# Kernel tuning notes

Hardware: AMD Instinct MI355X
Metric: run time of the kernel (lower is better)

Reference implementation:

```python
import jax, jax.numpy as jnp
import numpy as np

N = 60000      # total nodes
D = 300        # feature dim
R = 5          # num relations == num bases
E = 1_000_000  # edges
S = 25000      # last_idx_senses
G = 50000      # last_idx_globals
BATCH = 32


def setup_inputs() -> dict:
    key = jax.random.key(0)
    ks = jax.random.split(key, 12)
    x = jax.random.normal(ks[0], (N, D), dtype=jnp.float32)
    edge_index = jax.random.randint(ks[1], (2, E), 0, N, dtype=jnp.int32)
    edge_type = jax.random.randint(ks[2], (E,), 0, R, dtype=jnp.int32)
    current_node_index = jax.random.randint(ks[3], (BATCH,), 0, N, dtype=jnp.int32)
    scale = 1.0 / np.sqrt(D)
    # RGCNConv basis decomposition params (num_bases == num_relations)
    basis = jax.random.normal(ks[4], (R, D, D), dtype=jnp.float32) * scale
    comp = jax.random.normal(ks[5], (R, R), dtype=jnp.float32) * scale
    root = jax.random.normal(ks[6], (D, D), dtype=jnp.float32) * scale
    bias = jnp.zeros((D,), dtype=jnp.float32)
    # heads
    w_global = jax.random.normal(ks[7], (G - S, D), dtype=jnp.float32) * scale
    b_global = jnp.zeros((G - S,), dtype=jnp.float32)
    w_sense = jax.random.normal(ks[8], (S, D), dtype=jnp.float32) * scale
    b_sense = jnp.zeros((S,), dtype=jnp.float32)
    return {
        "x": x, "edge_index": edge_index, "edge_type": edge_type,
        "current_node_index": current_node_index,
        "basis": basis, "comp": comp, "root": root, "bias": bias,
        "w_global": w_global, "b_global": b_global,
        "w_sense": w_sense, "b_sense": b_sense,
    }


def reference(x, edge_index, edge_type, current_node_index,
              basis, comp, root, bias,
              w_global, b_global, w_sense, b_sense):
    src, dst = edge_index[0], edge_index[1]
    # Combined segment id over (dst node, relation): mean-aggregate source
    # features per (node, relation), then apply the per-relation transform
    # (mean(x_j) @ W_r == mean(x_j @ W_r); matches PyG RGCNConv aggr='mean').
    seg = dst * R + edge_type                      # [E]
    msg_sum = jax.ops.segment_sum(x[src], seg, num_segments=N * R)  # [N*R, D]
    cnt = jax.ops.segment_sum(jnp.ones((E,), jnp.float32), seg, num_segments=N * R)
    mean = msg_sum.reshape(N, R, D) / jnp.maximum(cnt.reshape(N, R, 1), 1.0)
    # basis decomposition: W_r = sum_b comp[r,b] * basis[b]
    W = jnp.einsum('rb,bij->rij', comp, basis)     # [R, D, D]
    agg = jnp.einsum('nrd,rde->ne', mean, W)       # [N, D]
    h = jax.nn.relu(agg + x @ root + bias)         # [N, D]
    hc = h[current_node_index]                     # [B, D]
    logits_global = hc @ w_global.T + b_global     # [B, G-S]
    logits_sense = hc @ w_sense.T + b_sense        # [B, S]
    return (jax.nn.log_softmax(logits_global, axis=-1),
            jax.nn.log_softmax(logits_sense, axis=-1))
```

## Files before the change

### kernel.cpp

```cpp
#include <hip/hip_runtime.h>
#include <hip/hip_bf16.h>
#include <math.h>

#define NN 60000
#define D 300
#define R 5
#define NE 1000000
#define B 32
#define NG 25000
#define NS 25000
#define NROWS 50000
#define KCH 50
#define NKC 36
#define HCP 304
#define MCAP 1000000

typedef __bf16 bf16x8 __attribute__((ext_vector_type(8)));
typedef float f32x16 __attribute__((ext_vector_type(16)));


__global__ void zero_ws(float4* __restrict__ p) {
    int i = blockIdx.x * 256 + threadIdx.x;
    if (i < 12040) p[i] = float4{0.f, 0.f, 0.f, 0.f};
    if (i == 0) ((int*)p)[53024] = 0;
}

__global__ __launch_bounds__(256) void edge_scan2(
        const int* __restrict__ ei, const int* __restrict__ et,
        const int* __restrict__ cur,
        float* __restrict__ wcnt, int2* __restrict__ mlist, int* __restrict__ mcnt) {
    __shared__ unsigned int tbl[32];
    __shared__ int curl[B];
    int tid = threadIdx.x;
    if (tid < 32) tbl[tid] = 0u;
    __syncthreads();
    if (tid < B) {
        int c = cur[tid];
        curl[tid] = c;
        atomicOr(&tbl[(c >> 5) & 31], 1u << (c & 31));
    }
    __syncthreads();
    long base = ((long)blockIdx.x * 256 + tid) * 4;
    if (base >= NE) return;
    int ds[4];
    if (base + 4 <= NE) {
        int4 d4 = *(const int4*)(ei + NE + base);
        ds[0] = d4.x; ds[1] = d4.y; ds[2] = d4.z; ds[3] = d4.w;
    } else {
        for (int k = 0; k < 4; ++k) ds[k] = (base + k < NE) ? ei[NE + base + k] : -1;
    }
    #pragma unroll
    for (int k = 0; k < 4; ++k) {
        int dst = ds[k];
        if (dst < 0) continue;
        if (!(tbl[(dst >> 5) & 31] & (1u << (dst & 31)))) continue;
        int e = (int)base + k;
        int r = -1, s = 0;
        for (int b = 0; b < B; ++b) {
            if (dst == curl[b]) {
                if (r < 0) { r = et[e]; s = ei[e]; }
                int slot = b * R + r;
                atomicAdd(&wcnt[slot], 1.0f);
                int pos = atomicAdd(mcnt, 1);
                if (pos < MCAP) mlist[pos] = int2{s, slot};
            }
        }
    }
}

__global__ __launch_bounds__(256) void edge_accum(
        const int2* __restrict__ mlist, const int* __restrict__ mcnt,
        const float* __restrict__ x, float* __restrict__ wsum) {
    int n = *mcnt; if (n > MCAP) n = MCAP;
    for (int m = blockIdx.x; m < n; m += gridDim.x) {
        int2 p = mlist[m];
        const float* xs = x + (long)p.x * D;
        float* sm = wsum + (long)p.y * D;
        for (int t = threadIdx.x; t < D; t += 256) atomicAdd(&sm[t], xs[t]);
    }
}

__global__ void stage_u(const float* __restrict__ x, const int* __restrict__ cur,
                        const float* __restrict__ comp,
                        const float* __restrict__ wsum, const float* __restrict__ wcnt,
                        float* __restrict__ U) {
    int b = blockIdx.x, t = threadIdx.x;
    __shared__ float cmp[R * R];
    __shared__ float inv[R];
    if (t < R * R) cmp[t] = comp[t];
    if (t < R) inv[t] = 1.0f / fmaxf(wcnt[b * R + t], 1.0f);
    __syncthreads();
    if (t >= D) return;
    int node = cur[b];
    U[(long)b * 1800 + t] = x[(long)node * D + t];
    float mean[R];
    #pragma unroll
    for (int r = 0; r < R; ++r) mean[r] = wsum[((long)b * R + r) * D + t] * inv[r];
    #pragma unroll
    for (int bb = 0; bb < R; ++bb) {
        float a = 0.f;
        #pragma unroll
        for (int r = 0; r < R; ++r) a = fmaf(cmp[r * R + bb], mean[r], a);
        U[(long)b * 1800 + 300 + bb * 300 + t] = a;
    }
}

__global__ __launch_bounds__(320) void rgcn_part(const float* __restrict__ root,
                                                 const float* __restrict__ basis,
                                                 const float* __restrict__ U,
                                                 float* __restrict__ part) {
    int kc = blockIdx.x, t = threadIdx.x;
    __shared__ float uL[B * KCH];
    int d0 = kc * KCH;
    for (int i = t; i < B * KCH; i += 320) {
        int b = i / KCH, dd = i - b * KCH;
        uL[i] = U[(long)b * 1800 + d0 + dd];
    }
    __syncthreads();
    if (t >= D) return;
    const float* Mbase = (d0 < 300) ? (root + (long)d0 * D) : (basis + (long)(d0 - 300) * D);
    float acc[B] = {};
    #pragma unroll 5
    for (int i = 0; i < KCH; ++i) {
        float m = Mbase[(long)i * D + t];
        #pragma unroll
        for (int b = 0; b < B; ++b) acc[b] = fmaf(uL[b * KCH + i], m, acc[b]);
    }
    for (int b = 0; b < B; ++b) part[((long)kc * B + b) * D + t] = acc[b];
}

__global__ void finish_hc(const float* __restrict__ part, const float* __restrict__ bias,
                          __bf16* __restrict__ hcb) {
    int b = blockIdx.x, t = threadIdx.x;
    if (t >= HCP) return;
    float a = 0.f;
    if (t < D) {
        a = bias[t];
        for (int kc = 0; kc < NKC; ++kc) a += part[((long)kc * B + b) * D + t];
        a = fmaxf(a, 0.f);
    }
    hcb[b * HCP + t] = (__bf16)a;
}

__global__ __launch_bounds__(64) void head_gemm_mfma(
    const __bf16* __restrict__ hcb, const float* __restrict__ wg, const float* __restrict__ bg,
    const float* __restrict__ wsn, const float* __restrict__ bsn, float* __restrict__ out) {
    int l = threadIdx.x;
    int j0 = blockIdx.x * 32;
    int lm = l & 31, lh = l >> 5;

    bf16x8 bfrag[19];
    const __bf16* hrow = hcb + lm * HCP + lh * 8;
    #pragma unroll
    for (int s = 0; s < 19; ++s) bfrag[s] = *(const bf16x8*)(hrow + 16 * s);

    int row = j0 + lm; if (row >= NROWS) row = NROWS - 1;
    const float* wrow = ((row < NG) ? (wg + (long)row * D) : (wsn + (long)(row - NG) * D)) + lh * 8;

    f32x16 acc = {};
    #pragma unroll
    for (int s = 0; s < 18; ++s) {
        float4 w0 = *(const float4*)(wrow + 16 * s);
        float4 w1 = *(const float4*)(wrow + 16 * s + 4);
        bf16x8 a;
        a[0] = (__bf16)w0.x; a[1] = (__bf16)w0.y; a[2] = (__bf16)w0.z; a[3] = (__bf16)w0.w;
        a[4] = (__bf16)w1.x; a[5] = (__bf16)w1.y; a[6] = (__bf16)w1.z; a[7] = (__bf16)w1.w;
        acc = __builtin_amdgcn_mfma_f32_32x32x16_bf16(a, bfrag[s], acc, 0, 0, 0);
    }
    {
        float4 w0, w1;
        if (lh == 0) {
            w0 = *(const float4*)(wrow + 288);
            w1 = *(const float4*)(wrow + 292);
        } else {
            w0 = *(const float4*)(wrow + 288);
            w1 = float4{0.f, 0.f, 0.f, 0.f};
        }
        bf16x8 a;
        a[0] = (__bf16)w0.x; a[1] = (__bf16)w0.y; a[2] = (__bf16)w0.z; a[3] = (__bf16)w0.w;
        a[4] = (__bf16)w1.x; a[5] = (__bf16)w1.y; a[6] = (__bf16)w1.z; a[7] = (__bf16)w1.w;
        acc = __builtin_amdgcn_mfma_f32_32x32x16_bf16(a, bfrag[18], acc, 0, 0, 0);
    }

    int b = lm;
    #pragma unroll
    for (int r = 0; r < 16; ++r) {
        int j = j0 + (r & 3) + 8 * (r >> 2) + 4 * lh;
        if (j >= NROWS) continue;
        float bv = (j < NG) ? bg[j] : bsn[j - NG];
        float* op = (j < NG) ? (out + (long)b * NG + j)
                             : (out + (long)B * NG + (long)b * NS + (j - NG));
        *op = acc[r] + bv;
    }
}

__global__ __launch_bounds__(1024) void log_softmax_rows(float* __restrict__ out) {
    int row = blockIdx.x;
    int head = row >> 5, b = row & 31;
    float* p = out + (long)head * (B * NG) + (long)b * NG;
    float4* p4 = (float4*)p;
    int tid = threadIdx.x;
    __shared__ float red[16];
    float m = -INFINITY;
    for (int i = tid; i < 6250; i += 1024) {
        float4 v = p4[i];
        m = fmaxf(fmaxf(fmaxf(m, v.x), v.y), fmaxf(v.z, v.w));
    }
    #pragma unroll
    for (int o = 32; o; o >>= 1) m = fmaxf(m, __shfl_xor(m, o));
    if ((tid & 63) == 0) red[tid >> 6] = m;
    __syncthreads();
    if (tid == 0) {
        float mm = red[0];
        for (int i = 1; i < 16; ++i) mm = fmaxf(mm, red[i]);
        red[0] = mm;
    }
    __syncthreads();
    m = red[0];
    __syncthreads();
    float s = 0.f;
    for (int i = tid; i < 6250; i += 1024) {
        float4 v = p4[i];
        s += __expf(v.x - m) + __expf(v.y - m) + __expf(v.z - m) + __expf(v.w - m);
    }
    #pragma unroll
    for (int o = 32; o; o >>= 1) s += __shfl_xor(s, o);
    if ((tid & 63) == 0) red[tid >> 6] = s;
    __syncthreads();
    if (tid == 0) {
        float ss = 0.f;
        for (int i = 0; i < 16; ++i) ss += red[i];
        red[0] = m + __logf(ss);
    }
    __syncthreads();
    float lse = red[0];
    for (int i = tid; i < 6250; i += 1024) {
        float4 v = p4[i];
        v.x -= lse; v.y -= lse; v.z -= lse; v.w -= lse;
        p4[i] = v;
    }
}

extern "C" void kernel_launch(void* const* d_in, const int* in_sizes, int n_in,
                              void* d_out, int out_size, void* d_ws, size_t ws_size,
                              hipStream_t stream) {
    const float* x     = (const float*)d_in[0];
    const int*   ei    = (const int*)d_in[1];
    const int*   et    = (const int*)d_in[2];
    const int*   cur   = (const int*)d_in[3];
    const float* basis = (const float*)d_in[4];
    const float* comp  = (const float*)d_in[5];
    const float* root  = (const float*)d_in[6];
    const float* bias  = (const float*)d_in[7];
    const float* wg    = (const float*)d_in[8];
    const float* bgl   = (const float*)d_in[9];
    const float* wsn   = (const float*)d_in[10];
    const float* bsn   = (const float*)d_in[11];
    float* out  = (float*)d_out;
    float* wsf  = (float*)d_ws;
    float* wsum = wsf;
    float* wcnt = wsf + 48000;
    __bf16* hcb = (__bf16*)(wsf + 48160);
    int*   mcnt = (int*)(wsf + 53024);
    int2*  mlist = (int2*)(wsf + 53028);
    float* part = out;
    float* U    = out + 400000;

    zero_ws<<<48, 256, 0, stream>>>((float4*)d_ws);
    edge_scan2<<<977, 256, 0, stream>>>(ei, et, cur, wcnt, mlist, mcnt);
    edge_accum<<<512, 256, 0, stream>>>(mlist, mcnt, x, wsum);
    stage_u<<<B, 320, 0, stream>>>(x, cur, comp, wsum, wcnt, U);
    rgcn_part<<<NKC, 320, 0, stream>>>(root, basis, U, part);
    finish_hc<<<B, 320, 0, stream>>>(part, bias, hcb);
    head_gemm_mfma<<<(NROWS + 31) / 32, 64, 0, stream>>>(hcb, wg, bgl, wsn, bsn, out);
    log_softmax_rows<<<64, 1024, 0, stream>>>(out);
}
```

Before: 75.97 us.

## Fuse edge scan with accumulation, merge RGCN stages, compute softmax stats in GEMM epilogue

The edge scan now keeps matching edges in a per-block shared list and accumulates their source rows straight away, which removes the global match list and the separate accumulate kernel. The mean/basis mixing, partial GEMM and final reduction are merged into one kernel. It reduces over blocks with float atomics and lets the last block finish the job, detected with a done counter. The head GEMM epilogue computes online max/sum partials per 32-column block, so the 1024-thread three-pass log-softmax becomes a small merge plus one subtract pass over many blocks. Kernel launches and full passes over the logits drop, in exchange for atomic contention and a per-block shared list capped at 64 entries that could silently drop edges.

```diff
diff --git a/kernel.cpp b/kernel.cpp
--- a/kernel.cpp
+++ b/kernel.cpp
@@ -10,10 +10,8 @@
 #define NG 25000
 #define NS 25000
 #define NROWS 50000
-#define KCH 50
-#define NKC 36
 #define HCP 304
-#define MCAP 1000000
+#define NBLK 1563
 
 typedef __bf16 bf16x8 __attribute__((ext_vector_type(8)));
 typedef float f32x16 __attribute__((ext_vector_type(16)));
@@ -21,18 +19,20 @@
 
 __global__ void zero_ws(float4* __restrict__ p) {
     int i = blockIdx.x * 256 + threadIdx.x;
-    if (i < 12040) p[i] = float4{0.f, 0.f, 0.f, 0.f};
-    if (i == 0) ((int*)p)[53024] = 0;
-}
-
-__global__ __launch_bounds__(256) void edge_scan2(
+    if (i < 14441) p[i] = float4{0.f, 0.f, 0.f, 0.f};
+}
+
+__global__ __launch_bounds__(256) void scan_accum(
         const int* __restrict__ ei, const int* __restrict__ et,
-        const int* __restrict__ cur,
-        float* __restrict__ wcnt, int2* __restrict__ mlist, int* __restrict__ mcnt) {
+        const int* __restrict__ cur, const float* __restrict__ x,
+        float* __restrict__ wsum, float* __restrict__ wcnt) {
     __shared__ unsigned int tbl[32];
     __shared__ int curl[B];
+    __shared__ int lcnt;
+    __shared__ int2 loc[64];
     int tid = threadIdx.x;
     if (tid < 32) tbl[tid] = 0u;
+    if (tid == 0) lcnt = 0;
     __syncthreads();
     if (tid < B) {
         int c = cur[tid];
@@ -41,110 +41,122 @@
     }
     __syncthreads();
     long base = ((long)blockIdx.x * 256 + tid) * 4;
-    if (base >= NE) return;
-    int ds[4];
-    if (base + 4 <= NE) {
-        int4 d4 = *(const int4*)(ei + NE + base);
-        ds[0] = d4.x; ds[1] = d4.y; ds[2] = d4.z; ds[3] = d4.w;
+    if (base < NE) {
+        int ds[4];
+        if (base + 4 <= NE) {
+            int4 d4 = *(const int4*)(ei + NE + base);
+            ds[0] = d4.x; ds[1] = d4.y; ds[2] = d4.z; ds[3] = d4.w;
+        } else {
+            for (int k = 0; k < 4; ++k) ds[k] = (base + k < NE) ? ei[NE + base + k] : -1;
+        }
+        #pragma unroll
+        for (int k = 0; k < 4; ++k) {
+            int dst = ds[k];
+            if (dst < 0) continue;
+            if (!(tbl[(dst >> 5) & 31] & (1u << (dst & 31)))) continue;
+            int e = (int)base + k;
+            int r = -1, s = 0;
+            for (int b = 0; b < B; ++b) {
+                if (dst == curl[b]) {
+                    if (r < 0) { r = et[e]; s = ei[e]; }
+                    int slot = b * R + r;
+                    atomicAdd(&wcnt[slot], 1.0f);
+                    int p = atomicAdd(&lcnt, 1);
+                    if (p < 64) loc[p] = int2{s, slot};
+                }
+            }
+        }
+    }
+    __syncthreads();
+    int n = lcnt; if (n > 64) n = 64;
+    for (int m = 0; m < n; ++m) {
+        int2 pr = loc[m];
+        const float* xs = x + (long)pr.x * D;
+        float* sm = wsum + (long)pr.y * D;
+        for (int t = tid; t < D; t += 256) atomicAdd(&sm[t], xs[t]);
+    }
+}
+
+__global__ __launch_bounds__(320) void rgcn_hc(
+        const float* __restrict__ x, const int* __restrict__ cur,
+        const float* __restrict__ comp, const float* __restrict__ root,
+        const float* __restrict__ basis, const float* __restrict__ bias,
+        const float* __restrict__ wsum, const float* __restrict__ wcnt,
+        float* __restrict__ hcf, int* __restrict__ done, __bf16* __restrict__ hcb) {
+    int kc = blockIdx.x, t = threadIdx.x;
+    __shared__ float uL[B * 50];
+    __shared__ float cmp[R * R];
+    __shared__ float inv[B * R];
+    __shared__ int curlS[B];
+    __shared__ int lastFlag;
+    if (t < R * R) cmp[t] = comp[t];
+    if (t < B * R) inv[t] = 1.0f / fmaxf(wcnt[t], 1.0f);
+    if (t < B) curlS[t] = cur[t];
+    __syncthreads();
+    int d0 = kc * 50;
+    if (kc < 6) {
+        for (int i = t; i < B * 50; i += 320) {
+            int b = i / 50, dd = i - b * 50;
+            uL[i] = x[(long)curlS[b] * D + d0 + dd];
+        }
     } else {
-        for (int k = 0; k < 4; ++k) ds[k] = (base + k < NE) ? ei[NE + base + k] : -1;
-    }
-    #pragma unroll
-    for (int k = 0; k < 4; ++k) {
-        int dst = ds[k];
-        if (dst < 0) continue;
-        if (!(tbl[(dst >> 5) & 31] & (1u << (dst & 31)))) continue;
-        int e = (int)base + k;
-        int r = -1, s = 0;
-        for (int b = 0; b < B; ++b) {
-            if (dst == curl[b]) {
-                if (r < 0) { r = et[e]; s = ei[e]; }
-                int slot = b * R + r;
-                atomicAdd(&wcnt[slot], 1.0f);
-                int pos = atomicAdd(mcnt, 1);
-                if (pos < MCAP) mlist[pos] = int2{s, slot};
-            }
-        }
-    }
-}
-
-__global__ __launch_bounds__(256) void edge_accum(
-        const int2* __restrict__ mlist, const int* __restrict__ mcnt,
-        const float* __restrict__ x, float* __restrict__ wsum) {
-    int n = *mcnt; if (n > MCAP) n = MCAP;
-    for (int m = blockIdx.x; m < n; m += gridDim.x) {
-        int2 p = mlist[m];
-        const float* xs = x + (long)p.x * D;
-        float* sm = wsum + (long)p.y * D;
-        for (int t = threadIdx.x; t < D; t += 256) atomicAdd(&sm[t], xs[t]);
-    }
-}
-
-__global__ void stage_u(const float* __restrict__ x, const int* __restrict__ cur,
-                        const float* __restrict__ comp,
-                        const float* __restrict__ wsum, const float* __restrict__ wcnt,
-                        float* __restrict__ U) {
-    int b = blockIdx.x, t = threadIdx.x;
-    __shared__ float cmp[R * R];
-    __shared__ float inv[R];
-    if (t < R * R) cmp[t] = comp[t];
-    if (t < R) inv[t] = 1.0f / fmaxf(wcnt[b * R + t], 1.0f);
-    __syncthreads();
-    if (t >= D) return;
-    int node = cur[b];
-    U[(long)b * 1800 + t] = x[(long)node * D + t];
-    float mean[R];
-    #pragma unroll
-    for (int r = 0; r < R; ++r) mean[r] = wsum[((long)b * R + r) * D + t] * inv[r];
-    #pragma unroll
-    for (int bb = 0; bb < R; ++bb) {
+        int g0 = d0 - 300;
+        int bb = g0 / 300, t0 = g0 - bb * 300;
+        for (int i = t; i < B * 50; i += 320) {
+            int b = i / 50, dd = i - b * 50;
+            float a = 0.f;
+            #pragma unroll
+            for (int r = 0; r < R; ++r)
+                a = fmaf(cmp[r * R + bb] * inv[b * R + r], wsum[((long)b * R + r) * D + t0 + dd], a);
+            uL[i] = a;
+        }
+    }
+    __syncthreads();
+    const float* Mb = (kc < 6) ? (root + (long)d0 * D) : (basis + (long)(d0 - 300) * D);
+    if (t < D) {
+        float acc[B] = {};
+        #pragma unroll 5
+        for (int i = 0; i < 50; ++i) {
+            float m = Mb[(long)i * D + t];
+            #pragma unroll
+            for (int b = 0; b < B; ++b) acc[b] = fmaf(uL[b * 50 + i], m, acc[b]);
+        }
+        for (int b = 0; b < B; ++b) atomicAdd(&hcf[b * D + t], acc[b]);
+    }
+    __syncthreads();
+    if (t == 0) {
+        __threadfence();
+        int p = atomicAdd(done, 1);
+        lastFlag = (p == 35);
+    }
+    __syncthreads();
+    if (!lastFlag) return;
+    __threadfence();
+    for (int i = t; i < B * HCP; i += 320) {
+        int b = i / HCP, tt = i - b * HCP;
         float a = 0.f;
-        #pragma unroll
-        for (int r = 0; r < R; ++r) a = fmaf(cmp[r * R + bb], mean[r], a);
-        U[(long)b * 1800 + 300 + bb * 300 + t] = a;
-    }
-}
-
-__global__ __launch_bounds__(320) void rgcn_part(const float* __restrict__ root,
-                                                 const float* __restrict__ basis,
-                                                 const float* __restrict__ U,
-                                                 float* __restrict__ part) {
-    int kc = blockIdx.x, t = threadIdx.x;
-    __shared__ float uL[B * KCH];
-    int d0 = kc * KCH;
-    for (int i = t; i < B * KCH; i += 320) {
-        int b = i / KCH, dd = i - b * KCH;
-        uL[i] = U[(long)b * 1800 + d0 + dd];
-    }
-    __syncthreads();
-    if (t >= D) return;
-    const float* Mbase = (d0 < 300) ? (root + (long)d0 * D) : (basis + (long)(d0 - 300) * D);
-    float acc[B] = {};
-    #pragma unroll 5
-    for (int i = 0; i < KCH; ++i) {
-        float m = Mbase[(long)i * D + t];
-        #pragma unroll
-        for (int b = 0; b < B; ++b) acc[b] = fmaf(uL[b * KCH + i], m, acc[b]);
-    }
-    for (int b = 0; b < B; ++b) part[((long)kc * B + b) * D + t] = acc[b];
-}
-
-__global__ void finish_hc(const float* __restrict__ part, const float* __restrict__ bias,
-                          __bf16* __restrict__ hcb) {
-    int b = blockIdx.x, t = threadIdx.x;
-    if (t >= HCP) return;
-    float a = 0.f;
-    if (t < D) {
-        a = bias[t];
-        for (int kc = 0; kc < NKC; ++kc) a += part[((long)kc * B + b) * D + t];
-        a = fmaxf(a, 0.f);
-    }
-    hcb[b * HCP + t] = (__bf16)a;
+        if (tt < D) {
+            a = atomicAdd(&hcf[b * D + tt], 0.0f) + bias[tt];
+            a = fmaxf(a, 0.f);
+        }
+        hcb[i] = (__bf16)a;
+    }
+}
+
+__device__ inline void online_upd(float& m, float& s, float v) {
+    if (v > m) { s = s * __expf(m - v) + 1.0f; m = v; }
+    else       { s += __expf(v - m); }
+}
+__device__ inline void online_merge(float& m, float& s, float om, float os) {
+    float M = fmaxf(m, om);
+    s = s * __expf(m - M) + os * __expf(om - M);
+    m = M;
 }
 
 __global__ __launch_bounds__(64) void head_gemm_mfma(
     const __bf16* __restrict__ hcb, const float* __restrict__ wg, const float* __restrict__ bg,
-    const float* __restrict__ wsn, const float* __restrict__ bsn, float* __restrict__ out) {
+    const float* __restrict__ wsn, const float* __restrict__ bsn,
+    float* __restrict__ out, float2* __restrict__ pm2) {
     int l = threadIdx.x;
     int j0 = blockIdx.x * 32;
     int lm = l & 31, lh = l >> 5;
@@ -183,61 +195,59 @@
     }
 
     int b = lm;
+    float m0 = -3.0e38f, s0 = 0.f, m1 = -3.0e38f, s1 = 0.f;
     #pragma unroll
     for (int r = 0; r < 16; ++r) {
         int j = j0 + (r & 3) + 8 * (r >> 2) + 4 * lh;
         if (j >= NROWS) continue;
         float bv = (j < NG) ? bg[j] : bsn[j - NG];
+        float v = acc[r] + bv;
         float* op = (j < NG) ? (out + (long)b * NG + j)
                              : (out + (long)B * NG + (long)b * NS + (j - NG));
-        *op = acc[r] + bv;
-    }
-}
-
-__global__ __launch_bounds__(1024) void log_softmax_rows(float* __restrict__ out) {
-    int row = blockIdx.x;
-    int head = row >> 5, b = row & 31;
-    float* p = out + (long)head * (B * NG) + (long)b * NG;
-    float4* p4 = (float4*)p;
+        *op = v;
+        if (j < NG) online_upd(m0, s0, v); else online_upd(m1, s1, v);
+    }
+    float om0 = __shfl_xor(m0, 32), os0 = __shfl_xor(s0, 32);
+    float om1 = __shfl_xor(m1, 32), os1 = __shfl_xor(s1, 32);
+    online_merge(m0, s0, om0, os0);
+    online_merge(m1, s1, om1, os1);
+    if (lh == 0) {
+        pm2[(long)b * NBLK + blockIdx.x]       = float2{m0, s0};
+        pm2[(long)(B + b) * NBLK + blockIdx.x] = float2{m1, s1};
+    }
+}
+
+__global__ __launch_bounds__(256) void sub_lse(float* __restrict__ out,
+                                               const float2* __restrict__ pm2) {
+    int row = blockIdx.x / 25, c = blockIdx.x % 25;
     int tid = threadIdx.x;
-    __shared__ float red[16];
-    float m = -INFINITY;
-    for (int i = tid; i < 6250; i += 1024) {
-        float4 v = p4[i];
-        m = fmaxf(fmaxf(fmaxf(m, v.x), v.y), fmaxf(v.z, v.w));
-    }
-    #pragma unroll
-    for (int o = 32; o; o >>= 1) m = fmaxf(m, __shfl_xor(m, o));
-    if ((tid & 63) == 0) red[tid >> 6] = m;
+    const float2* pr = pm2 + (long)row * NBLK;
+    float m = -3.0e38f, s = 0.f;
+    for (int i = tid; i < NBLK; i += 256) {
+        float2 e = pr[i];
+        online_merge(m, s, e.x, e.y);
+    }
+    #pragma unroll
+    for (int o = 32; o; o >>= 1) {
+        float om = __shfl_xor(m, o), os = __shfl_xor(s, o);
+        online_merge(m, s, om, os);
+    }
+    __shared__ float sm[4], ss[4];
+    __shared__ float lseS;
+    if ((tid & 63) == 0) { sm[tid >> 6] = m; ss[tid >> 6] = s; }
     __syncthreads();
     if (tid == 0) {
-        float mm = red[0];
-        for (int i = 1; i < 16; ++i) mm = fmaxf(mm, red[i]);
-        red[0] = mm;
-    }
-    __syncthreads();
-    m = red[0];
-    __syncthreads();
-    float s = 0.f;
-    for (int i = tid; i < 6250; i += 1024) {
-        float4 v = p4[i];
-        s += __expf(v.x - m) + __expf(v.y - m) + __expf(v.z - m) + __expf(v.w - m);
-    }
-    #pragma unroll
-    for (int o = 32; o; o >>= 1) s += __shfl_xor(s, o);
-    if ((tid & 63) == 0) red[tid >> 6] = s;
-    __syncthreads();
-    if (tid == 0) {
-        float ss = 0.f;
-        for (int i = 0; i < 16; ++i) ss += red[i];
-        red[0] = m + __logf(ss);
-    }
-    __syncthreads();
-    float lse = red[0];
-    for (int i = tid; i < 6250; i += 1024) {
-        float4 v = p4[i];
+        float M = sm[0], S = ss[0];
+        for (int w = 1; w < 4; ++w) online_merge(M, S, sm[w], ss[w]);
+        lseS = M + __logf(S);
+    }
+    __syncthreads();
+    float lse = lseS;
+    float4* o4 = (float4*)out + (long)row * 6250 + c * 250;
+    if (tid < 250) {
+        float4 v = o4[tid];
         v.x -= lse; v.y -= lse; v.z -= lse; v.w -= lse;
-        p4[i] = v;
+        o4[tid] = v;
     }
 }
 
@@ -258,20 +268,16 @@
     const float* bsn   = (const float*)d_in[11];
     float* out  = (float*)d_out;
     float* wsf  = (float*)d_ws;
-    float* wsum = wsf;
-    float* wcnt = wsf + 48000;
-    __bf16* hcb = (__bf16*)(wsf + 48160);
-    int*   mcnt = (int*)(wsf + 53024);
-    int2*  mlist = (int2*)(wsf + 53028);
-    float* part = out;
-    float* U    = out + 400000;
-
-    zero_ws<<<48, 256, 0, stream>>>((float4*)d_ws);
-    edge_scan2<<<977, 256, 0, stream>>>(ei, et, cur, wcnt, mlist, mcnt);
-    edge_accum<<<512, 256, 0, stream>>>(mlist, mcnt, x, wsum);
-    stage_u<<<B, 320, 0, stream>>>(x, cur, comp, wsum, wcnt, U);
-    rgcn_part<<<NKC, 320, 0, stream>>>(root, basis, U, part);
-    finish_hc<<<B, 320, 0, stream>>>(part, bias, hcb);
-    head_gemm_mfma<<<(NROWS + 31) / 32, 64, 0, stream>>>(hcb, wg, bgl, wsn, bsn, out);
-    log_softmax_rows<<<64, 1024, 0, stream>>>(out);
-}
+    float* wsum  = wsf;
+    float* wcnt  = wsf + 48000;
+    float* hcf   = wsf + 48160;
+    int*   done  = (int*)(wsf + 57760);
+    __bf16* hcb  = (__bf16*)(wsf + 57764);
+    float2* pm2  = (float2*)(wsf + 62628);
+
+    zero_ws<<<57, 256, 0, stream>>>((float4*)d_ws);
+    scan_accum<<<977, 256, 0, stream>>>(ei, et, cur, x, wsum, wcnt);
+    rgcn_hc<<<36, 320, 0, stream>>>(x, cur, comp, root, basis, bias, wsum, wcnt, hcf, done, hcb);
+    head_gemm_mfma<<<NBLK, 64, 0, stream>>>(hcb, wg, bgl, wsn, bsn, out, pm2);
+    sub_lse<<<1600, 256, 0, stream>>>(out, pm2);
+}
```

Result: slower. 81.70 us (+7.5%).
